# Performance work log

Measured on AMD Instinct MI355X. Metric: run time of the kernel, lower is better.

## Reference

```python
import jax, jax.numpy as jnp
import numpy as np

EPS = 1e-9
ROUTING_ITERS = 3


def _squash_elem(s):
    # Faithful to source: squash over trailing axis of size 1 => elementwise.
    sq = s * s
    return (sq / (1.0 + sq)) * s / jnp.sqrt(sq + EPS)


def setup_inputs() -> dict:
    key = jax.random.key(0)
    k1, k2 = jax.random.split(key)
    B, I, P = 16, 2048, 16   # batch, num_input_capsules, input_dim_capsules
    O, D = 64, 32            # num_capsules, dim_capsules
    x = jax.random.normal(k1, (B, I, P), dtype=jnp.float32)
    # glorot-ish scale for the transformation weights
    W = jax.random.normal(k2, (1, I, O, D, P), dtype=jnp.float32) * (1.0 / np.sqrt(P))
    bias = jnp.zeros((1, 1, O, D, 1), dtype=jnp.float32)
    return {"x": x, "W": W, "bias": bias}


def reference(x, W, bias):
    # u_hat[b,i,o,d] = sum_p W[0,i,o,d,p] * x[b,i,p]  (the tile+mul+reduce in TF)
    u_hat = jnp.einsum('bip,iodp->biod', x, W[0])
    B, I, O, _ = u_hat.shape
    bias_od = bias[0, 0, :, :, 0]               # [O, D]
    b_logits = jnp.zeros((B, I, O), dtype=u_hat.dtype)
    v = None
    for it in range(ROUTING_ITERS):
        c = jax.nn.softmax(b_logits, axis=2)     # softmax over output capsules
        s = jnp.einsum('bio,biod->bod', c, u_hat) + bias_od
        v = _squash_elem(s)                      # [B, O, D]
        if it < ROUTING_ITERS - 1:
            # agreement[b,i,o] = sum_d u_hat[b,i,o,d] * v[b,o,d]
            b_logits = b_logits + jnp.einsum('biod,bod->bio', u_hat, v)
    return v  # [B, num_capsules, dim_capsules]
```

## Files before the change

### kernel.cpp

```cpp
#include <hip/hip_runtime.h>

#define B_ 16
#define I_ 2048
#define OD_ 2048
#define EPSQ 1e-9f

typedef float v4f __attribute__((ext_vector_type(4)));

__device__ __forceinline__ float squashf(float s) {
  float sq = s * s;
  return sq / (1.0f + sq) * s * rsqrtf(sq + EPSQ);
}

__global__ __launch_bounds__(256, 4) void k_uhat(
    const float* __restrict__ x, const float* __restrict__ W,
    float* __restrict__ u, float* __restrict__ part0)
{
  const int t = threadIdx.x;
  const int q = blockIdx.x & 3;
  const int ic = blockIdx.x >> 2;
  const int i0 = ic * 8;
  const int pr = q * 256 + t;

  float s0a[B_], s0b[B_];
#pragma unroll
  for (int b = 0; b < B_; ++b) { s0a[b] = 0.f; s0b[b] = 0.f; }

  for (int ii = 0; ii < 8; ++ii) {
    const int i = i0 + ii;
    const v4f* wp = (const v4f*)(W + (size_t)(i * OD_ + pr * 2) * 16);
    v4f w[8];
#pragma unroll
    for (int k = 0; k < 8; ++k) w[k] = __builtin_nontemporal_load(wp + k);

#pragma unroll
    for (int b = 0; b < B_; ++b) {
      const v4f* xp = (const v4f*)(x + (size_t)(b * I_ + i) * 16);
      float u0 = 0.f, u1 = 0.f;
#pragma unroll
      for (int qq = 0; qq < 4; ++qq) {
        v4f xq = xp[qq];
        v4f wa = w[qq], wb = w[qq + 4];
        u0 += xq.x * wa.x + xq.y * wa.y + xq.z * wa.z + xq.w * wa.w;
        u1 += xq.x * wb.x + xq.y * wb.y + xq.z * wb.z + xq.w * wb.w;
      }
      float2 uv; uv.x = u0; uv.y = u1;
      *(float2*)(u + (size_t)(b * I_ + i) * OD_ + pr * 2) = uv;
      s0a[b] += u0; s0b[b] += u1;
    }
  }
#pragma unroll
  for (int b = 0; b < B_; ++b) {
    float2 sv; sv.x = s0a[b]; sv.y = s0b[b];
    ((float2*)part0)[(size_t)(ic * B_ + b) * 1024 + pr] = sv;
  }
}

__global__ __launch_bounds__(256) void k_s0red(
    const float* __restrict__ part0, float* __restrict__ s0)
{
  const int b = blockIdx.x >> 3;
  const int od = (blockIdx.x & 7) * 256 + threadIdx.x;
  float a = 0.f;
  const float* p = part0 + (size_t)b * OD_ + od;
#pragma unroll 8
  for (int ic = 0; ic < 256; ++ic) a += p[(size_t)ic * B_ * OD_];
  s0[b * OD_ + od] = a;
}

__global__ __launch_bounds__(64, 2) void k_route(
    const float* __restrict__ u,
    const float* __restrict__ sA, float scaleA,
    const float* __restrict__ sB,
    const float* __restrict__ bias,
    float* __restrict__ part)
{
  const int o = threadIdx.x;
  const int b = blockIdx.x >> 7;
  const int g = blockIdx.x & 127;
  const int i0 = g * 16;

  v4f vv[8], acc[8];
  {
    const float* sa = sA + b * OD_ + o * 32;
    const float* sb = sB ? sB + b * OD_ + o * 32 : nullptr;
    const float* bp = bias + o * 32;
#pragma unroll
    for (int qq = 0; qq < 8; ++qq) {
#pragma unroll
      for (int j = 0; j < 4; ++j) {
        float bs = bp[qq * 4 + j];
        float val = squashf(sa[qq * 4 + j] * scaleA + bs);
        if (sb) val += squashf(sb[qq * 4 + j] + bs);
        vv[qq][j] = val;
      }
      v4f z = {0.f, 0.f, 0.f, 0.f};
      acc[qq] = z;
    }
  }

  for (int ii = 0; ii < 16; ++ii) {
    const int i = i0 + ii;
    const v4f* up = (const v4f*)(u + (size_t)(b * I_ + i) * OD_ + o * 32);
    v4f r[8];
#pragma unroll
    for (int qq = 0; qq < 8; ++qq) r[qq] = up[qq];

    float logit = 0.f;
#pragma unroll
    for (int qq = 0; qq < 8; ++qq)
#pragma unroll
      for (int j = 0; j < 4; ++j)
        logit = fmaf(r[qq][j], vv[qq][j], logit);

    float m = logit;
#pragma unroll
    for (int off = 32; off > 0; off >>= 1) m = fmaxf(m, __shfl_xor(m, off, 64));
    float e = __expf(logit - m);
    float sm = e;
#pragma unroll
    for (int off = 32; off > 0; off >>= 1) sm += __shfl_xor(sm, off, 64);
    float c = e * __builtin_amdgcn_rcpf(sm);

#pragma unroll
    for (int qq = 0; qq < 8; ++qq)
#pragma unroll
      for (int j = 0; j < 4; ++j)
        acc[qq][j] = fmaf(c, r[qq][j], acc[qq][j]);
  }

  v4f* pp = (v4f*)(part + (size_t)(b * 128 + g) * OD_ + o * 32);
#pragma unroll
  for (int qq = 0; qq < 8; ++qq) pp[qq] = acc[qq];
}

__global__ __launch_bounds__(256) void k_s1red(
    const float* __restrict__ part, float* __restrict__ s1)
{
  const int b = blockIdx.x >> 3;
  const int od = (blockIdx.x & 7) * 256 + threadIdx.x;
  float a = 0.f;
  const float* p = part + (size_t)b * 128 * OD_ + od;
#pragma unroll 8
  for (int g = 0; g < 128; ++g) a += p[(size_t)g * OD_];
  s1[b * OD_ + od] = a;
}

__global__ __launch_bounds__(256) void k_outred(
    const float* __restrict__ part, const float* __restrict__ bias,
    float* __restrict__ out)
{
  const int b = blockIdx.x >> 3;
  const int od = (blockIdx.x & 7) * 256 + threadIdx.x;
  float a = 0.f;
  const float* p = part + (size_t)b * 128 * OD_ + od;
#pragma unroll 8
  for (int g = 0; g < 128; ++g) a += p[(size_t)g * OD_];
  out[b * OD_ + od] = squashf(a + bias[od]);
}

extern "C" void kernel_launch(void* const* d_in, const int* in_sizes, int n_in,
                              void* d_out, int out_size, void* d_ws, size_t ws_size,
                              hipStream_t stream) {
  const float* x = (const float*)d_in[0];
  const float* W = (const float*)d_in[1];
  const float* bias = (const float*)d_in[2];
  float* out = (float*)d_out;

  char* ws = (char*)d_ws;
  float* u_ws  = (float*)ws;
  float* part0 = (float*)(ws + 268435456ull);
  float* part1 = (float*)(ws + 301989888ull);
  float* part2 = part0;
  float* s0    = (float*)(ws + 318767104ull);
  float* s1    = s0 + 32768;

  k_uhat <<<dim3(1024), dim3(256), 0, stream>>>(x, W, u_ws, part0);
  k_s0red<<<dim3(128),  dim3(256), 0, stream>>>(part0, s0);
  k_route<<<dim3(2048), dim3(64),  0, stream>>>(u_ws, s0, 1.0f / 64.0f, nullptr, bias, part1);
  k_s1red<<<dim3(128),  dim3(256), 0, stream>>>(part1, s1);
  k_route<<<dim3(2048), dim3(64),  0, stream>>>(u_ws, s0, 1.0f / 64.0f, s1, bias, part2);
  k_outred<<<dim3(128), dim3(256), 0, stream>>>(part2, bias, out);
}
```

Before: 677.9 us.

## Stage x in LDS, prefetch W, and regroup routing into multi-wave blocks

k_uhat now has each thread own a single od column. The block's x slice is staged in shared memory, and the next capsule's W row is loaded while the current one is computed, replacing repeated global x loads with LDS reads. k_route moves from one-wave blocks over 16 capsules to four-wave blocks where each wave covers 8 capsules, which doubles the number of routing partial sums. The partial-sum reductions and workspace offsets are resized to match, at the cost of more partial-buffer traffic and longer reduction loops.

Result: no change. 680.9 us (+0.5%).

```diff
diff --git a/kernel.cpp b/kernel.cpp
--- a/kernel.cpp
+++ b/kernel.cpp
@@ -12,48 +12,65 @@
   return sq / (1.0f + sq) * s * rsqrtf(sq + EPSQ);
 }
 
+__device__ __forceinline__ float dot4(v4f a, v4f b) {
+  return a.x * b.x + a.y * b.y + a.z * b.z + a.w * b.w;
+}
+
 __global__ __launch_bounds__(256, 4) void k_uhat(
     const float* __restrict__ x, const float* __restrict__ W,
     float* __restrict__ u, float* __restrict__ part0)
 {
+  __shared__ float xs[8 * 16 * 16];
   const int t = threadIdx.x;
-  const int q = blockIdx.x & 3;
-  const int ic = blockIdx.x >> 2;
+  const int e = blockIdx.x & 7;
+  const int ic = blockIdx.x >> 3;
   const int i0 = ic * 8;
-  const int pr = q * 256 + t;
-
-  float s0a[B_], s0b[B_];
-#pragma unroll
-  for (int b = 0; b < B_; ++b) { s0a[b] = 0.f; s0b[b] = 0.f; }
+  const int od = e * 256 + t;
+
+  {
+    const int b = t >> 4, j = t & 15;
+    const float4* src = (const float4*)(x + (size_t)(b * I_ + i0) * 16);
+    float4 a0 = src[j * 2], a1 = src[j * 2 + 1];
+    const int ii = j >> 1, pq = (j & 1) * 2;
+    float4* dst = (float4*)xs + ii * 64 + b * 4;
+    dst[pq] = a0; dst[pq + 1] = a1;
+  }
+  __syncthreads();
+
+  float s0acc[B_];
+#pragma unroll
+  for (int b = 0; b < B_; ++b) s0acc[b] = 0.f;
+
+  const v4f* wb = (const v4f*)(W + ((size_t)i0 * OD_ + od) * 16);
+  v4f wc[4], wn[4];
+#pragma unroll
+  for (int k = 0; k < 4; ++k) wc[k] = __builtin_nontemporal_load(wb + k);
 
   for (int ii = 0; ii < 8; ++ii) {
-    const int i = i0 + ii;
-    const v4f* wp = (const v4f*)(W + (size_t)(i * OD_ + pr * 2) * 16);
-    v4f w[8];
-#pragma unroll
-    for (int k = 0; k < 8; ++k) w[k] = __builtin_nontemporal_load(wp + k);
-
+    if (ii < 7) {
+      const v4f* wnp = wb + (size_t)(ii + 1) * 8192;
+#pragma unroll
+      for (int k = 0; k < 4; ++k) wn[k] = __builtin_nontemporal_load(wnp + k);
+    }
+    const v4f* xv = (const v4f*)xs + ii * 64;
+    float* up = u + (size_t)(i0 + ii) * OD_ + od;
 #pragma unroll
     for (int b = 0; b < B_; ++b) {
-      const v4f* xp = (const v4f*)(x + (size_t)(b * I_ + i) * 16);
-      float u0 = 0.f, u1 = 0.f;
-#pragma unroll
-      for (int qq = 0; qq < 4; ++qq) {
-        v4f xq = xp[qq];
-        v4f wa = w[qq], wb = w[qq + 4];
-        u0 += xq.x * wa.x + xq.y * wa.y + xq.z * wa.z + xq.w * wa.w;
-        u1 += xq.x * wb.x + xq.y * wb.y + xq.z * wb.z + xq.w * wb.w;
-      }
-      float2 uv; uv.x = u0; uv.y = u1;
-      *(float2*)(u + (size_t)(b * I_ + i) * OD_ + pr * 2) = uv;
-      s0a[b] += u0; s0b[b] += u1;
-    }
-  }
-#pragma unroll
-  for (int b = 0; b < B_; ++b) {
-    float2 sv; sv.x = s0a[b]; sv.y = s0b[b];
-    ((float2*)part0)[(size_t)(ic * B_ + b) * 1024 + pr] = sv;
-  }
+      v4f x0 = xv[b * 4 + 0], x1 = xv[b * 4 + 1];
+      v4f x2 = xv[b * 4 + 2], x3 = xv[b * 4 + 3];
+      float s = dot4(x0, wc[0]) + dot4(x1, wc[1]) +
+                dot4(x2, wc[2]) + dot4(x3, wc[3]);
+      up[(size_t)b * I_ * OD_] = s;
+      s0acc[b] += s;
+    }
+    if (ii < 7) {
+#pragma unroll
+      for (int k = 0; k < 4; ++k) wc[k] = wn[k];
+    }
+  }
+#pragma unroll
+  for (int b = 0; b < B_; ++b)
+    part0[((size_t)ic * B_ + b) * OD_ + od] = s0acc[b];
 }
 
 __global__ __launch_bounds__(256) void k_s0red(
@@ -68,17 +85,19 @@
   s0[b * OD_ + od] = a;
 }
 
-__global__ __launch_bounds__(64, 2) void k_route(
+__global__ __launch_bounds__(256, 4) void k_route(
     const float* __restrict__ u,
     const float* __restrict__ sA, float scaleA,
     const float* __restrict__ sB,
     const float* __restrict__ bias,
     float* __restrict__ part)
 {
-  const int o = threadIdx.x;
-  const int b = blockIdx.x >> 7;
-  const int g = blockIdx.x & 127;
-  const int i0 = g * 16;
+  const int t = threadIdx.x;
+  const int o = t & 63;
+  const int wv = t >> 6;
+  const int b = blockIdx.x >> 6;
+  const int g = (blockIdx.x & 63) * 4 + wv;
+  const int i0 = g * 8;
 
   v4f vv[8], acc[8];
   {
@@ -99,7 +118,7 @@
     }
   }
 
-  for (int ii = 0; ii < 16; ++ii) {
+  for (int ii = 0; ii < 8; ++ii) {
     const int i = i0 + ii;
     const v4f* up = (const v4f*)(u + (size_t)(b * I_ + i) * OD_ + o * 32);
     v4f r[8];
@@ -116,11 +135,11 @@
     float m = logit;
 #pragma unroll
     for (int off = 32; off > 0; off >>= 1) m = fmaxf(m, __shfl_xor(m, off, 64));
-    float e = __expf(logit - m);
-    float sm = e;
+    float ex = __expf(logit - m);
+    float sm = ex;
 #pragma unroll
     for (int off = 32; off > 0; off >>= 1) sm += __shfl_xor(sm, off, 64);
-    float c = e * __builtin_amdgcn_rcpf(sm);
+    float c = ex * __builtin_amdgcn_rcpf(sm);
 
 #pragma unroll
     for (int qq = 0; qq < 8; ++qq)
@@ -129,7 +148,7 @@
         acc[qq][j] = fmaf(c, r[qq][j], acc[qq][j]);
   }
 
-  v4f* pp = (v4f*)(part + (size_t)(b * 128 + g) * OD_ + o * 32);
+  v4f* pp = (v4f*)(part + (size_t)(b * 256 + g) * OD_ + o * 32);
 #pragma unroll
   for (int qq = 0; qq < 8; ++qq) pp[qq] = acc[qq];
 }
@@ -140,9 +159,9 @@
   const int b = blockIdx.x >> 3;
   const int od = (blockIdx.x & 7) * 256 + threadIdx.x;
   float a = 0.f;
-  const float* p = part + (size_t)b * 128 * OD_ + od;
+  const float* p = part + (size_t)b * 256 * OD_ + od;
 #pragma unroll 8
-  for (int g = 0; g < 128; ++g) a += p[(size_t)g * OD_];
+  for (int g = 0; g < 256; ++g) a += p[(size_t)g * OD_];
   s1[b * OD_ + od] = a;
 }
 
@@ -153,9 +172,9 @@
   const int b = blockIdx.x >> 3;
   const int od = (blockIdx.x & 7) * 256 + threadIdx.x;
   float a = 0.f;
-  const float* p = part + (size_t)b * 128 * OD_ + od;
+  const float* p = part + (size_t)b * 256 * OD_ + od;
 #pragma unroll 8
-  for (int g = 0; g < 128; ++g) a += p[(size_t)g * OD_];
+  for (int g = 0; g < 256; ++g) a += p[(size_t)g * OD_];
   out[b * OD_ + od] = squashf(a + bias[od]);
 }
 
@@ -172,13 +191,13 @@
   float* part0 = (float*)(ws + 268435456ull);
   float* part1 = (float*)(ws + 301989888ull);
   float* part2 = part0;
-  float* s0    = (float*)(ws + 318767104ull);
+  float* s0    = (float*)(ws + 335544320ull);
   float* s1    = s0 + 32768;
 
-  k_uhat <<<dim3(1024), dim3(256), 0, stream>>>(x, W, u_ws, part0);
+  k_uhat <<<dim3(2048), dim3(256), 0, stream>>>(x, W, u_ws, part0);
   k_s0red<<<dim3(128),  dim3(256), 0, stream>>>(part0, s0);
-  k_route<<<dim3(2048), dim3(64),  0, stream>>>(u_ws, s0, 1.0f / 64.0f, nullptr, bias, part1);
+  k_route<<<dim3(1024), dim3(256), 0, stream>>>(u_ws, s0, 1.0f / 64.0f, nullptr, bias, part1);
   k_s1red<<<dim3(128),  dim3(256), 0, stream>>>(part1, s1);
-  k_route<<<dim3(2048), dim3(64),  0, stream>>>(u_ws, s0, 1.0f / 64.0f, s1, bias, part2);
+  k_route<<<dim3(1024), dim3(256), 0, stream>>>(u_ws, s0, 1.0f / 64.0f, s1, bias, part2);
   k_outred<<<dim3(128), dim3(256), 0, stream>>>(part2, bias, out);
 }
```
